# Kernel tuning notes

Measured on AMD Instinct MI355X. Metric: run time of the kernel, lower is better.

The kernel has to match this reference:

```python
import jax, jax.numpy as jnp
import numpy as np

NH = 32      # num_attention_heads
HD = 128     # head dim (kv_channels)
NG = 2       # multi_query_group_num
LAYER_NUMBER = 1


def apply_rotary_pos_emb(x, rope_cache):
    # x: [b, np, sq, hn]; rope_cache: [1, sq_max, rot/2, 2]
    b, nh, sq, hn = x.shape
    rot_dim = rope_cache.shape[-2] * 2
    xr, x_pass = x[..., :rot_dim], x[..., rot_dim:]
    xs = xr.reshape(b, nh, sq, rot_dim // 2, 2)
    c = rope_cache[:, :sq].reshape(-1, 1, sq, rot_dim // 2, 2)
    out = jnp.stack(
        [xs[..., 0] * c[..., 0] - xs[..., 1] * c[..., 1],
         xs[..., 1] * c[..., 0] + xs[..., 0] * c[..., 1]], axis=-1)
    out = out.reshape(b, nh, sq, rot_dim)
    return jnp.concatenate([out, x_pass], axis=-1)


def setup_inputs() -> dict:
    key = jax.random.key(0)
    ks = jax.random.split(key, 5)
    b, sq, h = 2, 2048, 4096
    qkv_out = NH * HD + 2 * NG * HD  # 4608
    return {
        "hidden_states": jax.random.normal(ks[0], (b, sq, h), jnp.float32),
        "rope_cache": jax.random.normal(ks[1], (1, sq, HD // 4, 2), jnp.float32),
        "W_qkv": jax.random.normal(ks[2], (h, qkv_out), jnp.float32) * 0.02,
        "b_qkv": jax.random.normal(ks[3], (qkv_out,), jnp.float32) * 0.02,
        "W_dense": jax.random.normal(ks[4], (NH * HD, h), jnp.float32) * 0.02,
    }


def reference(hidden_states, rope_cache, W_qkv, b_qkv, W_dense):
    b, sq, h = hidden_states.shape
    mixed = hidden_states @ W_qkv + b_qkv  # [b, sq, nh*hd + 2*ng*hd]
    q_sz = NH * HD
    kv_sz = NG * HD
    q = mixed[..., :q_sz].reshape(b, sq, NH, HD).transpose(0, 2, 1, 3)          # [b,nh,sq,hd]
    k = mixed[..., q_sz:q_sz + kv_sz].reshape(b, sq, NG, HD).transpose(0, 2, 1, 3)  # [b,ng,sq,hd]
    v = mixed[..., q_sz + kv_sz:].reshape(b, sq, NG, HD).transpose(0, 2, 1, 3)      # [b,ng,sq,hd]

    q = apply_rotary_pos_emb(q, rope_cache)
    k = apply_rotary_pos_emb(k, rope_cache)

    # expand KV groups to full heads (multi-query attention)
    rep = NH // NG
    k = jnp.broadcast_to(k[:, :, None], (b, NG, rep, sq, HD)).reshape(b, NH, sq, HD)
    v = jnp.broadcast_to(v[:, :, None], (b, NG, rep, sq, HD)).reshape(b, NH, sq, HD)

    # CoreAttention (eager path, fp32 softmax, causal)
    coeff = float(max(1, LAYER_NUMBER))  # apply_query_key_layer_scaling
    norm_factor = np.sqrt(HD) * coeff
    scores = jnp.einsum("bhqd,bhkd->bhqk", q, k) / norm_factor
    scores = scores.astype(jnp.float32) * coeff
    causal = jnp.tril(jnp.ones((sq, sq), dtype=bool))
    scores = jnp.where(causal[None, None], scores, -jnp.inf)
    probs = jax.nn.softmax(scores, axis=-1).astype(v.dtype)
    context = jnp.einsum("bhqk,bhkd->bhqd", probs, v)   # [b,nh,sq,hd]
    context = context.transpose(0, 2, 1, 3).reshape(b, sq, NH * HD)
    return context @ W_dense
```

## Files before the change

### kernel.cpp

```cpp
#include <hip/hip_runtime.h>
#include <hip/hip_bf16.h>
#include <stdint.h>

#define B_    2
#define SQ    2048
#define H_    4096
#define NHEAD 32
#define HDIM  128
#define NGRP  2
#define QKVN  4608
#define SCALE 0.08838834764831845f
#define QSCALE (0.08838834764831845f * 1.4426950408889634f)

typedef __attribute__((ext_vector_type(8))) short bf16x8;
typedef __attribute__((ext_vector_type(4))) short bf16x4;
typedef __attribute__((ext_vector_type(4))) float f32x4;

__device__ __forceinline__ float b2f(short s) {
  union { float f; unsigned u; } x; x.u = ((unsigned)(unsigned short)s) << 16; return x.f;
}
__device__ __forceinline__ short f2b(float f) {
  union { float f; unsigned u; } x; x.f = f;
  unsigned r = x.u + 0x7fffu + ((x.u >> 16) & 1u);
  return (short)(r >> 16);
}
__device__ __forceinline__ void gll16(const void* g, void* l) {
  __builtin_amdgcn_global_load_lds(
      (const __attribute__((address_space(1))) unsigned int*)g,
      (__attribute__((address_space(3))) unsigned int*)l, 16, 0, 0);
}

__global__ void conv_f32_bf16(const float* __restrict__ x, short* __restrict__ y, int n) {
  int i = (blockIdx.x * blockDim.x + threadIdx.x) * 4;
  if (i >= n) return;
  float4 v = *(const float4*)(x + i);
  union { short s[4]; uint2 u; } o;
  o.s[0] = f2b(v.x); o.s[1] = f2b(v.y); o.s[2] = f2b(v.z); o.s[3] = f2b(v.w);
  *(uint2*)(y + i) = o.u;
}

__global__ void transpose_f32_bf16(const float* __restrict__ W, short* __restrict__ Wt,
                                   int R, int C) {
  __shared__ float tile[32][33];
  int c0 = blockIdx.x * 32, r0 = blockIdx.y * 32;
  int tx = threadIdx.x, ty = threadIdx.y;
  #pragma unroll
  for (int i = 0; i < 32; i += 8)
    tile[ty + i][tx] = W[(size_t)(r0 + ty + i) * C + c0 + tx];
  __syncthreads();
  #pragma unroll
  for (int i = 0; i < 32; i += 8)
    Wt[(size_t)(c0 + ty + i) * R + r0 + tx] = f2b(tile[tx][ty + i]);
}

template<bool BIAS, bool OUTF32>
__global__ __launch_bounds__(256, 2) void gemm_bf16(
    const short* __restrict__ A, const short* __restrict__ Bt,
    const float* __restrict__ bias, short* __restrict__ outb,
    float* __restrict__ outf, int M, int N, int K)
{
  __shared__ short smA[128 * 64];
  __shared__ short smB[128 * 64];
  const int t = threadIdx.x;
  const int l = t & 63;
  const int w = t >> 6;
  const int wr = w >> 1, wc = w & 1;
  const int m0 = blockIdx.y * 128, n0 = blockIdx.x * 128;

  const f32x4 z = {0.f, 0.f, 0.f, 0.f};
  f32x4 acc[4][4];
  #pragma unroll
  for (int m = 0; m < 4; ++m)
    #pragma unroll
    for (int n = 0; n < 4; ++n) acc[m][n] = z;

  for (int k0 = 0; k0 < K; k0 += 64) {
    __syncthreads();
    #pragma unroll
    for (int i = 0; i < 4; ++i) {
      int c = t + i * 256;
      int row = c >> 3, slot = c & 7;
      int ss = slot ^ (row & 7);
      gll16(A  + (size_t)(m0 + row) * K + k0 + ss * 8,
            (char*)smA + (i * 256 + w * 64) * 16);
      gll16(Bt + (size_t)(n0 + row) * K + k0 + ss * 8,
            (char*)smB + (i * 256 + w * 64) * 16);
    }
    __syncthreads();
    #pragma unroll
    for (int kk = 0; kk < 2; ++kk) {
      bf16x8 a[4], b[4];
      #pragma unroll
      for (int m = 0; m < 4; ++m) {
        int row = wr * 64 + m * 16 + (l & 15);
        int off = (kk * 64 + ((l >> 4) << 4)) ^ ((row & 7) << 4);
        a[m] = *(const bf16x8*)((const char*)smA + row * 128 + off);
      }
      #pragma unroll
      for (int n = 0; n < 4; ++n) {
        int row = wc * 64 + n * 16 + (l & 15);
        int off = (kk * 64 + ((l >> 4) << 4)) ^ ((row & 7) << 4);
        b[n] = *(const bf16x8*)((const char*)smB + row * 128 + off);
      }
      #pragma unroll
      for (int m = 0; m < 4; ++m)
        #pragma unroll
        for (int n = 0; n < 4; ++n)
          acc[m][n] = __builtin_amdgcn_mfma_f32_16x16x32_bf16(a[m], b[n], acc[m][n], 0, 0, 0);
    }
  }

  #pragma unroll
  for (int m = 0; m < 4; ++m) {
    int row = m0 + wr * 64 + m * 16 + ((l >> 4) << 2);
    #pragma unroll
    for (int n = 0; n < 4; ++n) {
      int col = n0 + wc * 64 + n * 16 + (l & 15);
      float bv = BIAS ? bias[col] : 0.f;
      #pragma unroll
      for (int j = 0; j < 4; ++j) {
        float vv = acc[m][n][j] + bv;
        if (OUTF32) outf[(size_t)(row + j) * N + col] = vv;
        else        outb[(size_t)(row + j) * N + col] = f2b(vv);
      }
    }
  }
}

__global__ void rope_split(const short* __restrict__ mixed, const float* __restrict__ rope,
                           short* __restrict__ qo, short* __restrict__ ko, short* __restrict__ vo)
{
  const int CH = QKVN / 8;
  int idx = blockIdx.x * blockDim.x + threadIdx.x;
  if (idx >= B_ * SQ * CH) return;
  int row = idx / CH;
  int cc = (idx - row * CH) * 8;
  int b = row >> 11, s = row & 2047;

  bf16x8 xv = *(const bf16x8*)(mixed + (size_t)row * QKVN + cc);
  float x[8];
  #pragma unroll
  for (int i = 0; i < 8; ++i) x[i] = b2f(xv[i]);

  int sect, hh, d = cc & 127;
  if (cc < 4096)      { sect = 0; hh = cc >> 7; }
  else if (cc < 4352) { sect = 1; hh = (cc - 4096) >> 7; }
  else                { sect = 2; hh = (cc - 4352) >> 7; }

  if (sect < 2 && d < 64) {
    float4 ca = *(const float4*)(rope + s * 64 + d);
    float4 cb = *(const float4*)(rope + s * 64 + d + 4);
    float t0;
    t0 = x[0]*ca.x - x[1]*ca.y; x[1] = x[1]*ca.x + x[0]*ca.y; x[0] = t0;
    t0 = x[2]*ca.z - x[3]*ca.w; x[3] = x[3]*ca.z + x[2]*ca.w; x[2] = t0;
    t0 = x[4]*cb.x - x[5]*cb.y; x[5] = x[5]*cb.x + x[4]*cb.y; x[4] = t0;
    t0 = x[6]*cb.z - x[7]*cb.w; x[7] = x[7]*cb.z + x[6]*cb.w; x[6] = t0;
  }
  if (sect == 0) {
    #pragma unroll
    for (int i = 0; i < 8; ++i) x[i] *= QSCALE;
  }

  short* dst; size_t oidx;
  if (sect == 0)      { dst = qo; oidx = (((size_t)(b * NHEAD + hh) * SQ) + s) * HDIM + d; }
  else if (sect == 1) { dst = ko; oidx = (((size_t)(b * NGRP + hh) * SQ) + s) * HDIM + d; }
  else                { dst = vo; oidx = (((size_t)(b * NGRP + hh) * SQ) + s) * HDIM + d; }
  bf16x8 ov;
  #pragma unroll
  for (int i = 0; i < 8; ++i) ov[i] = f2b(x[i]);
  *(bf16x8*)(dst + oidx) = ov;
}

__global__ __launch_bounds__(512, 2) void attn_fwd(
    const short* __restrict__ q, const short* __restrict__ k,
    const short* __restrict__ v, short* __restrict__ ctx)
{
  __shared__ short smem[8192 + 9216];
  short* smK = smem;
  short* smV = smem + 8192;

  const int h = blockIdx.y, b = blockIdx.z;
  const int g = h >> 4;
  const int t = threadIdx.x, l = t & 63, w = t >> 6;
  const int lq = l & 15, hi = l >> 4;

  const short* qbase = q + ((size_t)(b * NHEAD + h) * SQ) * HDIM;
  const short* kbase = k + ((size_t)(b * NGRP + g) * SQ) * HDIM;
  const short* vbase = v + ((size_t)(b * NGRP + g) * SQ) * HDIM;

  const f32x4 z = {0.f, 0.f, 0.f, 0.f};

  for (int pass = 0; pass < 2; ++pass) {
    const int s = pass ? (7 - (int)blockIdx.x) : (int)blockIdx.x;
    const int q0 = s * 256;
    const int qw = q0 + w * 32;
    const int nkt = 4 * s + 4;

    bf16x8 qf[2][4];
    #pragma unroll
    for (int fq = 0; fq < 2; ++fq)
      #pragma unroll
      for (int kf = 0; kf < 4; ++kf)
        qf[fq][kf] = *(const bf16x8*)(qbase + (size_t)(qw + fq * 16 + lq) * HDIM + kf * 32 + hi * 8);

    f32x4 of[2][8];
    #pragma unroll
    for (int a = 0; a < 2; ++a)
      #pragma unroll
      for (int d = 0; d < 8; ++d) of[a][d] = z;
    float mrow[2] = {-1e30f, -1e30f};
    float lrow[2] = {0.f, 0.f};

    for (int kt = 0; kt < nkt; ++kt) {
      const int kb = kt * 64;
      __syncthreads();
      #pragma unroll
      for (int i = 0; i < 2; ++i) {
        int c = t + i * 512;
        int row = c >> 4, slot = c & 15;
        int ss = slot ^ (row & 7);
        gll16(kbase + (size_t)(kb + row) * HDIM + ss * 8,
              (char*)smK + (i * 512 + w * 64) * 16);
      }
      #pragma unroll
      for (int i = 0; i < 2; ++i) {
        int c = t + i * 512;
        int key = c & 63, d0 = (c >> 6) << 3;
        bf16x8 vv = *(const bf16x8*)(vbase + (size_t)(kb + key) * HDIM + d0);
        #pragma unroll
        for (int jj = 0; jj < 8; ++jj)
          smV[(d0 + jj) * 72 + key] = vv[jj];
      }
      __syncthreads();

      if (kb > qw + 31) continue;

      f32x4 st[2][4];
      #pragma unroll
      for (int fq = 0; fq < 2; ++fq)
        #pragma unroll
        for (int fk = 0; fk < 4; ++fk) st[fq][fk] = z;
      #pragma unroll
      for (int kf = 0; kf < 4; ++kf) {
        bf16x8 kfr[4];
        #pragma unroll
        for (int fk = 0; fk < 4; ++fk) {
          int row = fk * 16 + lq;
          int slot = (kf * 4 + hi) ^ (row & 7);
          kfr[fk] = *(const bf16x8*)((const char*)smK + row * 256 + slot * 16);
        }
        #pragma unroll
        for (int fq = 0; fq < 2; ++fq)
          #pragma unroll
          for (int fk = 0; fk < 4; ++fk)
            st[fq][fk] = __builtin_amdgcn_mfma_f32_16x16x32_bf16(kfr[fk], qf[fq][kf], st[fq][fk], 0, 0, 0);
      }

      bf16x4 pa[2][4];
      #pragma unroll
      for (int fq = 0; fq < 2; ++fq) {
        float sv[16];
        #pragma unroll
        for (int fk = 0; fk < 4; ++fk)
          #pragma unroll
          for (int j = 0; j < 4; ++j) sv[fk * 4 + j] = st[fq][fk][j];
        if (kb + 63 > qw + fq * 16) {
          int qrow = qw + fq * 16 + lq;
          #pragma unroll
          for (int fk = 0; fk < 4; ++fk)
            #pragma unroll
            for (int j = 0; j < 4; ++j)
              if (kb + fk * 16 + hi * 4 + j > qrow) sv[fk * 4 + j] = -1e30f;
        }
        float mx = sv[0];
        #pragma unroll
        for (int i = 1; i < 16; ++i) mx = fmaxf(mx, sv[i]);
        mx = fmaxf(mx, __shfl_xor(mx, 16));
        mx = fmaxf(mx, __shfl_xor(mx, 32));
        if (__any(mx > mrow[fq] + 11.0f)) {
          float mn = fmaxf(mrow[fq], mx);
          float corr = exp2f(mrow[fq] - mn);
          mrow[fq] = mn;
          lrow[fq] *= corr;
          float cj[4];
          #pragma unroll
          for (int j = 0; j < 4; ++j) cj[j] = __shfl(corr, hi * 4 + j);
          #pragma unroll
          for (int df = 0; df < 8; ++df)
            #pragma unroll
            for (int j = 0; j < 4; ++j) of[fq][df][j] *= cj[j];
        }
        float rs = 0.f;
        #pragma unroll
        for (int i = 0; i < 16; ++i) { sv[i] = exp2f(sv[i] - mrow[fq]); rs += sv[i]; }
        rs += __shfl_xor(rs, 16);
        rs += __shfl_xor(rs, 32);
        lrow[fq] += rs;
        #pragma unroll
        for (int fk = 0; fk < 4; ++fk) {
          bf16x4 p;
          p[0] = f2b(sv[fk * 4 + 0]); p[1] = f2b(sv[fk * 4 + 1]);
          p[2] = f2b(sv[fk * 4 + 2]); p[3] = f2b(sv[fk * 4 + 3]);
          pa[fq][fk] = p;
        }
      }

      #pragma unroll
      for (int fk = 0; fk < 4; ++fk) {
        bf16x4 vb[8];
        #pragma unroll
        for (int df = 0; df < 8; ++df)
          vb[df] = *(const bf16x4*)(smV + (df * 16 + lq) * 72 + fk * 16 + hi * 4);
        #pragma unroll
        for (int df = 0; df < 8; ++df) {
          of[0][df] = __builtin_amdgcn_mfma_f32_16x16x16bf16_1k(pa[0][fk], vb[df], of[0][df], 0, 0, 0);
          of[1][df] = __builtin_amdgcn_mfma_f32_16x16x16bf16_1k(pa[1][fk], vb[df], of[1][df], 0, 0, 0);
        }
      }
    }

    #pragma unroll
    for (int fq = 0; fq < 2; ++fq) {
      float inv = 1.f / lrow[fq];
      float ij[4];
      #pragma unroll
      for (int j = 0; j < 4; ++j) ij[j] = __shfl(inv, hi * 4 + j);
      #pragma unroll
      for (int j = 0; j < 4; ++j) {
        int srow = qw + fq * 16 + hi * 4 + j;
        size_t rbase = ((size_t)(b * SQ + srow)) * (NHEAD * HDIM) + (size_t)h * HDIM;
        #pragma unroll
        for (int df = 0; df < 8; ++df)
          ctx[rbase + df * 16 + lq] = f2b(of[fq][df][j] * ij[j]);
      }
    }
    __syncthreads();
  }
}

extern "C" void kernel_launch(void* const* d_in, const int* in_sizes, int n_in,
                              void* d_out, int out_size, void* d_ws, size_t ws_size,
                              hipStream_t stream)
{
  const float* hidden = (const float*)d_in[0];
  const float* rope   = (const float*)d_in[1];
  const float* Wqkv   = (const float*)d_in[2];
  const float* bqkv   = (const float*)d_in[3];
  const float* Wd     = (const float*)d_in[4];
  float* out = (float*)d_out;

  if (ws_size < 113246208ULL) return;
  char* ws = (char*)d_ws;
  short* hsb   = (short*)(ws);
  short* wT    = (short*)(ws + 33554432);
  short* mixed = (short*)(ws + 71303168);
  short* k_r   = (short*)(ws + 109051904);
  short* v_r   = (short*)(ws + 111149056);

  conv_f32_bf16<<<16384, 256, 0, stream>>>(hidden, hsb, B_ * SQ * H_);
  transpose_f32_bf16<<<dim3(QKVN / 32, H_ / 32), dim3(32, 8), 0, stream>>>(Wqkv, wT, H_, QKVN);
  gemm_bf16<true, false><<<dim3(QKVN / 128, (B_ * SQ) / 128), 256, 0, stream>>>(
      hsb, wT, bqkv, mixed, nullptr, B_ * SQ, QKVN, H_);
  rope_split<<<9216, 256, 0, stream>>>(mixed, rope, hsb, k_r, v_r);
  transpose_f32_bf16<<<dim3(H_ / 32, H_ / 32), dim3(32, 8), 0, stream>>>(Wd, wT, H_, H_);
  attn_fwd<<<dim3(4, NHEAD, B_), 512, 0, stream>>>(hsb, k_r, v_r, mixed);
  gemm_bf16<false, true><<<dim3(H_ / 128, (B_ * SQ) / 128), 256, 0, stream>>>(
      mixed, wT, nullptr, nullptr, out, B_ * SQ, H_, H_);
}
```

Baseline: 539.2 us.

## Replace output projection GEMM with 256x256-tile pipelined MFMA kernel

Adds a new GEMM kernel with 256x256 output tiles, 512 threads, double-buffered LDS staged through direct global-to-LDS loads, XOR-swizzled LDS layout, interleaved staging and MFMA phases, and a grid swizzle for L2 locality. It replaces the 128x128-tile GEMM used for the dense output projection. The goal is more data reuse per tile and overlap of memory loads with matrix math. The cost is 128KB of LDS, a large accumulator register footprint, and hand-tuned waitcnt/barrier logic that could be fragile.

```diff
diff --git a/kernel.cpp b/kernel.cpp
--- a/kernel.cpp
+++ b/kernel.cpp
@@ -125,6 +125,113 @@
       }
     }
   }
+}
+
+__global__ __launch_bounds__(512, 2) void gemm256(
+    const short* __restrict__ A, const short* __restrict__ Bt,
+    float* __restrict__ outf, int M, int N, int K, int nbx)
+{
+  __shared__ char sm[131072];
+  const int t = threadIdx.x, l = t & 63, w = t >> 6;
+  const int lq = l & 15, hi = l >> 4;
+  const int wm = w >> 2, wn = w & 3;
+  const int nwg = (int)gridDim.x;
+  const int oid = (int)blockIdx.x;
+  const int swz = (oid & 7) * (nwg >> 3) + (oid >> 3);
+  const int by = swz / nbx, bx = swz - by * nbx;
+  const int m0 = by * 256, n0 = bx * 256;
+  const int nkt = K >> 6;
+
+  auto stage = [&](int tt, int r) {
+    int kb = (tt < nkt ? tt : tt - nkt) << 6;
+    const short* src = (r < 2) ? Bt + (size_t)(n0 + (r << 7)) * K + kb
+                               : A  + (size_t)(m0 + ((r - 2) << 7)) * K + kb;
+    char* dst = sm + ((tt & 1) << 16) + (r >= 2 ? 0 : 32768) + ((r & 1) << 14);
+    #pragma unroll
+    for (int i = 0; i < 2; ++i) {
+      int c = (i << 9) + t;
+      int row = c >> 3, ss = (c & 7) ^ (row & 7);
+      gll16(src + (size_t)row * K + ss * 8, dst + ((i << 9) + (w << 6)) * 16);
+    }
+  };
+  bf16x8 aC[2][2], bC[4][2];
+  auto ldA = [&](int b, int q, bf16x8 (&out)[2][2]) {
+    #pragma unroll
+    for (int fr = 0; fr < 2; ++fr) {
+      int ra = wm * 128 + q * 32 + fr * 16 + lq;
+      #pragma unroll
+      for (int kk = 0; kk < 2; ++kk)
+        out[fr][kk] = *(const bf16x8*)(sm + (b << 16) + ra * 128 + (((kk << 2) + hi) ^ (ra & 7)) * 16);
+    }
+  };
+  auto ldB = [&](int b, bf16x8 (&out)[4][2]) {
+    #pragma unroll
+    for (int fc = 0; fc < 4; ++fc) {
+      int rb = wn * 64 + fc * 16 + lq;
+      #pragma unroll
+      for (int kk = 0; kk < 2; ++kk)
+        out[fc][kk] = *(const bf16x8*)(sm + (b << 16) + 32768 + rb * 128 + (((kk << 2) + hi) ^ (rb & 7)) * 16);
+    }
+  };
+
+  const f32x4 z = {0.f, 0.f, 0.f, 0.f};
+  f32x4 acc[8][4];
+  #pragma unroll
+  for (int i = 0; i < 8; ++i)
+    #pragma unroll
+    for (int j = 0; j < 4; ++j) acc[i][j] = z;
+
+  stage(0, 0); stage(0, 1); stage(0, 2); stage(0, 3);
+  stage(1, 0); stage(1, 1); stage(1, 2);
+  asm volatile("s_waitcnt vmcnt(6)" ::: "memory");
+  __builtin_amdgcn_s_barrier();
+  ldB(0, bC); ldA(0, 0, aC);
+  asm volatile("s_waitcnt lgkmcnt(0)" ::: "memory");
+
+#define GPHASE(p, STG_T, STG_R)                                           \
+  {                                                                       \
+    stage((STG_T), (STG_R));                                              \
+    __builtin_amdgcn_sched_barrier(0);                                    \
+    __builtin_amdgcn_s_barrier();                                         \
+    __builtin_amdgcn_s_setprio(1);                                        \
+    _Pragma("unroll")                                                     \
+    for (int kk = 0; kk < 2; ++kk)                                        \
+      _Pragma("unroll")                                                   \
+      for (int fr = 0; fr < 2; ++fr)                                      \
+        _Pragma("unroll")                                                 \
+        for (int fc = 0; fc < 4; ++fc)                                    \
+          acc[(p) * 2 + fr][fc] = __builtin_amdgcn_mfma_f32_16x16x32_bf16(\
+              aC[fr][kk], bC[fc][kk], acc[(p) * 2 + fr][fc], 0, 0, 0);    \
+    __builtin_amdgcn_s_setprio(0);                                        \
+    if ((p) < 3) ldA(bsel, (p) + 1, aC);                                  \
+    else { ldA(bsel ^ 1, 0, aC); ldB(bsel ^ 1, bC); }                     \
+    asm volatile("s_waitcnt lgkmcnt(0)" ::: "memory");                    \
+    if ((p) == 2) asm volatile("s_waitcnt vmcnt(4)" ::: "memory");        \
+    __builtin_amdgcn_s_barrier();                                         \
+  }
+
+  for (int tt = 0; tt < nkt; ++tt) {
+    const int bsel = tt & 1;
+    GPHASE(0, tt + 1, 3)
+    GPHASE(1, tt + 2, 0)
+    GPHASE(2, tt + 2, 1)
+    GPHASE(3, tt + 2, 2)
+  }
+#undef GPHASE
+
+  #pragma unroll
+  for (int q = 0; q < 4; ++q)
+    #pragma unroll
+    for (int fr = 0; fr < 2; ++fr) {
+      int gr0 = m0 + wm * 128 + q * 32 + fr * 16 + hi * 4;
+      #pragma unroll
+      for (int fc = 0; fc < 4; ++fc) {
+        int col = n0 + wn * 64 + fc * 16 + lq;
+        #pragma unroll
+        for (int j = 0; j < 4; ++j)
+          outf[(size_t)(gr0 + j) * N + col] = acc[q * 2 + fr][fc][j];
+      }
+    }
 }
 
 __global__ void rope_split(const short* __restrict__ mixed, const float* __restrict__ rope,
@@ -364,6 +471,5 @@
   rope_split<<<9216, 256, 0, stream>>>(mixed, rope, hsb, k_r, v_r);
   transpose_f32_bf16<<<dim3(H_ / 32, H_ / 32), dim3(32, 8), 0, stream>>>(Wd, wT, H_, H_);
   attn_fwd<<<dim3(4, NHEAD, B_), 512, 0, stream>>>(hsb, k_r, v_r, mixed);
-  gemm_bf16<false, true><<<dim3(H_ / 128, (B_ * SQ) / 128), 256, 0, stream>>>(
-      mixed, wT, nullptr, nullptr, out, B_ * SQ, H_, H_);
-}
+  gemm256<<<256, 512, 0, stream>>>(mixed, wT, out, B_ * SQ, H_, H_, H_ / 256);
+}
```

Result: no change. 549.4 us (+1.9%).
